# Kernel tuning notes

Measured on AMD Instinct MI355X. Metric: run time of the kernel, lower is better.

The kernel has to match this reference:

```python
import jax, jax.numpy as jnp
import numpy as np

D = 256      # d_model
NH = 8       # num_heads
NP = 4       # n_points
H = 100      # feature map height (single level)
W = 100      # feature map width
B = 4
Q = H * W
S = H * W


def setup_inputs() -> dict:
    key = jax.random.key(0)
    ks = jax.random.split(key, 12)
    p = lambda k, shp, s=0.02: jax.random.normal(k, shp, jnp.float32) * s
    return {
        "hidden_states": jax.random.normal(ks[0], (B, Q, D), jnp.float32),
        "encoder_hidden_states": jax.random.normal(ks[1], (B, S, D), jnp.float32),
        "reference_points": jax.random.uniform(ks[2], (B, Q, 1, 2), jnp.float32),
        "spatial_shapes": jnp.array([[H, W]], dtype=jnp.int32),
        "W_off": p(ks[3], (NH * NP * 2, D)),
        "b_off": p(ks[4], (NH * NP * 2,), 0.5),
        "W_attn": p(ks[5], (NH * NP, D)),
        "b_attn": jnp.zeros((NH * NP,), jnp.float32),
        "W_val": p(ks[6], (D, D)),
        "b_val": jnp.zeros((D,), jnp.float32),
        "W_out": p(ks[7], (D, D)),
        "b_out": jnp.zeros((D,), jnp.float32),
    }


def _deform_attn(hidden_states, encoder_hidden_states, reference_points,
                 W_off, b_off, W_attn, b_attn, W_val, b_val, W_out, b_out):
    Bsz, Qn, Dm = hidden_states.shape
    d = Dm // NH

    # value projection -> [B, NH, S, d]
    value = (encoder_hidden_states @ W_val.T + b_val).reshape(Bsz, S, NH, d)
    vflat = value.transpose(0, 2, 1, 3).reshape(Bsz * NH, H * W, d)

    # sampling offsets [B,Q,NH,NP,2] (n_levels=1 squeezed)
    off = (hidden_states @ W_off.T + b_off).reshape(Bsz, Qn, NH, NP, 2)
    # attention weights softmax over (n_levels*n_points)=NP -> [B,Q,NH,NP]
    attn = jax.nn.softmax((hidden_states @ W_attn.T + b_attn).reshape(Bsz, Qn, NH, NP), axis=-1)

    # normalized sampling locations: ref + off / [W, H]
    normalizer = jnp.array([W, H], jnp.float32)
    # reference_points: [B,Q,1,2] (level dim) -> broadcast over heads/points
    loc = reference_points[:, :, None, 0, None, :] + off / normalizer  # [B,Q,NH,NP,2]

    # grid_sample semantics: grid = 2*loc - 1, align_corners=False, zeros padding
    gx = 2.0 * loc[..., 0] - 1.0
    gy = 2.0 * loc[..., 1] - 1.0
    x = ((gx + 1.0) * W - 1.0) * 0.5   # pixel coords [B,Q,NH,NP]
    y = ((gy + 1.0) * H - 1.0) * 0.5
    x0 = jnp.floor(x); y0 = jnp.floor(y)
    x1 = x0 + 1.0;     y1 = y0 + 1.0
    wx1 = x - x0; wx0 = 1.0 - wx1
    wy1 = y - y0; wy0 = 1.0 - wy1

    bh = jnp.arange(Bsz * NH)[:, None]

    def corner(xi, yi, wgt):
        valid = (xi >= 0) & (xi <= W - 1) & (yi >= 0) & (yi <= H - 1)
        xi_c = jnp.clip(xi, 0, W - 1).astype(jnp.int32)
        yi_c = jnp.clip(yi, 0, H - 1).astype(jnp.int32)
        idx = (yi_c * W + xi_c).transpose(0, 2, 1, 3).reshape(Bsz * NH, Qn * NP)
        g = vflat[bh, idx]  # [B*NH, Q*NP, d]
        wv = (wgt * valid.astype(wgt.dtype)).transpose(0, 2, 1, 3).reshape(Bsz * NH, Qn * NP, 1)
        return g * wv

    sampled = corner(x0, y0, wx0 * wy0)
    sampled = sampled + corner(x1, y0, wx1 * wy0)
    sampled = sampled + corner(x0, y1, wx0 * wy1)
    sampled = sampled + corner(x1, y1, wx1 * wy1)
    sampled = sampled.reshape(Bsz, NH, Qn, NP, d)

    out = jnp.einsum("bhqpd,bqhp->bqhd", sampled, attn).reshape(Bsz, Qn, Dm)
    return out @ W_out.T + b_out


def reference(hidden_states, encoder_hidden_states, reference_points, spatial_shapes,
              W_off, b_off, W_attn, b_attn, W_val, b_val, W_out, b_out):
    # spatial_shapes is static metadata (must equal [[H, W]]); shapes are baked in.
    return _deform_attn(hidden_states, encoder_hidden_states, reference_points,
                        W_off, b_off, W_attn, b_attn, W_val, b_val, W_out, b_out)
```

## Files before the change

kernel.cpp:

```cpp
#include <hip/hip_runtime.h>

constexpr int HH = 100;
constexpr int WW = 100;
constexpr int NH = 8;
constexpr int NP = 4;
constexpr int B  = 4;
constexpr int Q  = HH * WW;
constexpr int S  = Q;
constexpr int K  = 256;
constexpr int DH = 32;
constexpr int M  = B * Q;
constexpr int NTILES = M / 32;

typedef __attribute__((ext_vector_type(8))) short short8;
typedef __attribute__((ext_vector_type(4))) float f32x4;

struct __align__(8) ushort4p { unsigned short x, y, z, w; };

__device__ inline unsigned short f2bf(float f) {
    unsigned u = __builtin_bit_cast(unsigned, f);
    u += 0x7fffu + ((u >> 16) & 1u);
    return (unsigned short)(u >> 16);
}
__device__ inline float bf2f(unsigned short h) {
    return __builtin_bit_cast(float, ((unsigned)h) << 16);
}
__device__ inline unsigned short f2h(float f) {
    _Float16 h = (_Float16)f;
    return __builtin_bit_cast(unsigned short, h);
}
__device__ inline float h2f(unsigned short u) {
    return (float)__builtin_bit_cast(_Float16, u);
}

__device__ inline void lds_st16s(short* base, int row, int stride, int kcol, short8 v) {
    *reinterpret_cast<short8*>(&base[row * stride + (kcol ^ ((row & 7) << 3))]) = v;
}
__device__ inline short8 lds_ld16s(const short* base, int row, int stride, int kcol) {
    return *reinterpret_cast<const short8*>(&base[row * stride + (kcol ^ ((row & 7) << 3))]);
}

__device__ inline short8 cvt8(float4 a, float4 b) {
    short8 r;
    r[0] = (short)f2bf(a.x); r[1] = (short)f2bf(a.y);
    r[2] = (short)f2bf(a.z); r[3] = (short)f2bf(a.w);
    r[4] = (short)f2bf(b.x); r[5] = (short)f2bf(b.y);
    r[6] = (short)f2bf(b.z); r[7] = (short)f2bf(b.w);
    return r;
}

__global__ __launch_bounds__(1024) void stage1(
    const float* __restrict__ enc, const float* __restrict__ Wval,
    const float* __restrict__ bval, unsigned short* __restrict__ vflat,
    const float* __restrict__ hidden, const float* __restrict__ Woff,
    const float* __restrict__ Wattn, const float* __restrict__ boff,
    const float* __restrict__ battn, unsigned short* __restrict__ proj)
{
    __shared__ __align__(16) short As[2][32 * 256];

    const int tid  = threadIdx.x;
    const int lane = tid & 63, w = tid >> 6;
    const int l15  = lane & 15, l4 = lane >> 4;
    const int arow = tid >> 5, ak = (tid & 31) * 8;

    constexpr int NV = 143, NJ = 113;

    if (blockIdx.x < NV) {
        const int n = w * 16 + l15;
        short8 breg[8];
#pragma unroll
        for (int ks = 0; ks < 8; ++ks) {
            const float* s = &Wval[(size_t)n * K + ks * 32 + l4 * 8];
            breg[ks] = cvt8(*reinterpret_cast<const float4*>(s),
                            *reinterpret_cast<const float4*>(s + 4));
        }
        const int nbase = w * 16 + l4 * 4;
        const float4 bias4 = *reinterpret_cast<const float4*>(&bval[nbase]);
        const int h = w >> 1;
        const int dd0 = nbase & 31;

        int t = blockIdx.x;
        float4 fa0, fa1;
        auto lda = [&](int tt) {
            const float* s = &enc[(size_t)(tt * 32 + arow) * K + ak];
            fa0 = *reinterpret_cast<const float4*>(s);
            fa1 = *reinterpret_cast<const float4*>(s + 4);
        };
        lda(t);
        lds_st16s(As[0], arow, 256, ak, cvt8(fa0, fa1));
        __syncthreads();
        int cur = 0;
        for (; t < NTILES; t += NV) {
            const bool more = (t + NV < NTILES);
            if (more) lda(t + NV);

            f32x4 acc0 = {0.f, 0.f, 0.f, 0.f}, acc1 = {0.f, 0.f, 0.f, 0.f};
#pragma unroll
            for (int ks = 0; ks < 8; ++ks) {
                const int kc = ks * 32 + l4 * 8;
                const short8 a0 = lds_ld16s(As[cur], l15, 256, kc);
                const short8 a1 = lds_ld16s(As[cur], 16 + l15, 256, kc);
                acc0 = __builtin_amdgcn_mfma_f32_16x16x32_bf16(breg[ks], a0, acc0, 0, 0, 0);
                acc1 = __builtin_amdgcn_mfma_f32_16x16x32_bf16(breg[ks], a1, acc1, 0, 0, 0);
            }
            const int m0 = t * 32;
            {
                const int m = m0 + l15;
                const int b_ = m / S, s_ = m - b_ * S;
                ushort4p pk;
                pk.x = f2bf(acc0[0] + bias4.x);
                pk.y = f2bf(acc0[1] + bias4.y);
                pk.z = f2bf(acc0[2] + bias4.z);
                pk.w = f2bf(acc0[3] + bias4.w);
                *reinterpret_cast<ushort4p*>(
                    &vflat[(((size_t)(b_ * NH + h)) * S + s_) * DH + dd0]) = pk;
            }
            {
                const int m = m0 + 16 + l15;
                const int b_ = m / S, s_ = m - b_ * S;
                ushort4p pk;
                pk.x = f2bf(acc1[0] + bias4.x);
                pk.y = f2bf(acc1[1] + bias4.y);
                pk.z = f2bf(acc1[2] + bias4.z);
                pk.w = f2bf(acc1[3] + bias4.w);
                *reinterpret_cast<ushort4p*>(
                    &vflat[(((size_t)(b_ * NH + h)) * S + s_) * DH + dd0]) = pk;
            }
            if (more) lds_st16s(As[cur ^ 1], arow, 256, ak, cvt8(fa0, fa1));
            __syncthreads();
            cur ^= 1;
        }
    } else {
        const int nf = w >> 1, mh = w & 1;
        const int n = nf * 16 + l15;
        short8 breg[8];
        float4 bias4 = {0.f, 0.f, 0.f, 0.f};
        const int nbase = nf * 16 + l4 * 4;
        if (w < 12) {
#pragma unroll
            for (int ks = 0; ks < 8; ++ks) {
                const float* s = (n < 64)
                    ? &Woff[(size_t)n * K + ks * 32 + l4 * 8]
                    : &Wattn[(size_t)(n - 64) * K + ks * 32 + l4 * 8];
                breg[ks] = cvt8(*reinterpret_cast<const float4*>(s),
                                *reinterpret_cast<const float4*>(s + 4));
            }
            bias4 = (nf < 4)
                ? *reinterpret_cast<const float4*>(&boff[nbase])
                : *reinterpret_cast<const float4*>(&battn[nbase - 64]);
        }

        int t = blockIdx.x - NV;
        float4 fa0, fa1;
        auto lda = [&](int tt) {
            const float* s = &hidden[(size_t)(tt * 32 + arow) * K + ak];
            fa0 = *reinterpret_cast<const float4*>(s);
            fa1 = *reinterpret_cast<const float4*>(s + 4);
        };
        lda(t);
        lds_st16s(As[0], arow, 256, ak, cvt8(fa0, fa1));
        __syncthreads();
        int cur = 0;
        for (; t < NTILES; t += NJ) {
            const bool more = (t + NJ < NTILES);
            if (more) lda(t + NJ);

            if (w < 12) {
                f32x4 acc = {0.f, 0.f, 0.f, 0.f};
#pragma unroll
                for (int ks = 0; ks < 8; ++ks) {
                    const int kc = ks * 32 + l4 * 8;
                    const short8 a = lds_ld16s(As[cur], mh * 16 + l15, 256, kc);
                    acc = __builtin_amdgcn_mfma_f32_16x16x32_bf16(breg[ks], a, acc, 0, 0, 0);
                }
                const int m = t * 32 + mh * 16 + l15;
                ushort4p pk;
                pk.x = f2h(acc[0] + bias4.x);
                pk.y = f2h(acc[1] + bias4.y);
                pk.z = f2h(acc[2] + bias4.z);
                pk.w = f2h(acc[3] + bias4.w);
                *reinterpret_cast<ushort4p*>(&proj[(size_t)m * 96 + nbase]) = pk;
            }
            if (more) lds_st16s(As[cur ^ 1], arow, 256, ak, cvt8(fa0, fa1));
            __syncthreads();
            cur ^= 1;
        }
    }
}

__global__ __launch_bounds__(256) void sample_agg(
    const unsigned short* __restrict__ vflat,
    const unsigned short* __restrict__ proj,
    const float* __restrict__ ref,
    unsigned short* __restrict__ tmp)
{
    const int nblk = gridDim.x;
    const int cpx  = nblk >> 3;
    const int swz  = (blockIdx.x & 7) * cpx + (blockIdx.x >> 3);

    const int lg   = threadIdx.x >> 2;
    const int lane = threadIdx.x & 3;
    const int d0   = lane * 8;

    const int g  = swz * 64 + lg;
    const int q  = g % Q;
    const int bh = g / Q;
    const int b  = bh >> 3;
    const int h  = bh & 7;

    const size_t bq = (size_t)b * Q + q;
    const float refx = ref[bq * 2 + 0];
    const float refy = ref[bq * 2 + 1];
    const unsigned short* pr = proj + bq * 96;

    float l[NP];
#pragma unroll
    for (int p = 0; p < NP; ++p) l[p] = h2f(pr[64 + h * 4 + p]);
    const float mx = fmaxf(fmaxf(l[0], l[1]), fmaxf(l[2], l[3]));
    float e[NP];
    float esum = 0.f;
#pragma unroll
    for (int p = 0; p < NP; ++p) { e[p] = __expf(l[p] - mx); esum += e[p]; }
    const float inv = 1.f / esum;

    const unsigned short* vbase = vflat + (size_t)bh * (S * DH);

    int   cidx[NP][4];
    float cw[NP][4];
#pragma unroll
    for (int p = 0; p < NP; ++p) {
        const float ox = h2f(pr[h * 8 + p * 2 + 0]);
        const float oy = h2f(pr[h * 8 + p * 2 + 1]);
        const float x = fmaf(refx, (float)WW, ox) - 0.5f;
        const float y = fmaf(refy, (float)HH, oy) - 0.5f;
        const float x0f = floorf(x), y0f = floorf(y);
        const float wx1 = x - x0f, wx0 = 1.f - wx1;
        const float wy1 = y - y0f, wy0 = 1.f - wy1;
        const int x0 = (int)x0f, y0 = (int)y0f;
        const bool vx0 = (x0 >= 0) && (x0 < WW);
        const bool vx1 = (x0 + 1 >= 0) && (x0 + 1 < WW);
        const bool vy0 = (y0 >= 0) && (y0 < HH);
        const bool vy1 = (y0 + 1 >= 0) && (y0 + 1 < HH);
        const int xi0 = min(max(x0, 0), WW - 1);
        const int xi1 = min(max(x0 + 1, 0), WW - 1);
        const int yi0 = min(max(y0, 0), HH - 1);
        const int yi1 = min(max(y0 + 1, 0), HH - 1);
        const float ap = e[p] * inv;
        cw[p][0] = ap * wx0 * wy0 * ((vx0 && vy0) ? 1.f : 0.f);
        cw[p][1] = ap * wx1 * wy0 * ((vx1 && vy0) ? 1.f : 0.f);
        cw[p][2] = ap * wx0 * wy1 * ((vx0 && vy1) ? 1.f : 0.f);
        cw[p][3] = ap * wx1 * wy1 * ((vx1 && vy1) ? 1.f : 0.f);
        cidx[p][0] = (yi0 * WW + xi0) * DH + d0;
        cidx[p][1] = (yi0 * WW + xi1) * DH + d0;
        cidx[p][2] = (yi1 * WW + xi0) * DH + d0;
        cidx[p][3] = (yi1 * WW + xi1) * DH + d0;
    }

    float o[8];
#pragma unroll
    for (int j = 0; j < 8; ++j) o[j] = 0.f;
#pragma unroll
    for (int p = 0; p < NP; ++p) {
#pragma unroll
        for (int c = 0; c < 4; ++c) {
            const short8 v = *reinterpret_cast<const short8*>(&vbase[cidx[p][c]]);
            const float wgt = cw[p][c];
#pragma unroll
            for (int j = 0; j < 8; ++j)
                o[j] = fmaf(wgt, bf2f((unsigned short)v[j]), o[j]);
        }
    }

    short8 ov;
#pragma unroll
    for (int j = 0; j < 8; ++j) ov[j] = (short)f2bf(o[j]);
    *reinterpret_cast<short8*>(&tmp[bq * 256 + h * 32 + d0]) = ov;
}

__global__ __launch_bounds__(1024) void out_proj(
    const unsigned short* __restrict__ tmp, const float* __restrict__ Wo,
    const float* __restrict__ bo, float* __restrict__ out)
{
    __shared__ __align__(16) short As[2][32 * 256];

    const int tid  = threadIdx.x;
    const int lane = tid & 63, w = tid >> 6;
    const int l15  = lane & 15, l4 = lane >> 4;
    const int arow = tid >> 5, ak = (tid & 31) * 8;

    const int n = w * 16 + l15;
    short8 breg[8];
#pragma unroll
    for (int ks = 0; ks < 8; ++ks) {
        const float* s = &Wo[(size_t)n * K + ks * 32 + l4 * 8];
        breg[ks] = cvt8(*reinterpret_cast<const float4*>(s),
                        *reinterpret_cast<const float4*>(s + 4));
    }
    const int nbase = w * 16 + l4 * 4;
    const float4 bias4 = *reinterpret_cast<const float4*>(&bo[nbase]);

    int t = blockIdx.x;
    short8 sa;
    auto lda = [&](int tt) {
        sa = *reinterpret_cast<const short8*>(&tmp[(size_t)(tt * 32 + arow) * K + ak]);
    };
    lda(t);
    lds_st16s(As[0], arow, 256, ak, sa);
    __syncthreads();
    int cur = 0;
    for (; t < NTILES; t += 256) {
        const bool more = (t + 256 < NTILES);
        if (more) lda(t + 256);

        f32x4 acc0 = {0.f, 0.f, 0.f, 0.f}, acc1 = {0.f, 0.f, 0.f, 0.f};
#pragma unroll
        for (int ks = 0; ks < 8; ++ks) {
            const int kc = ks * 32 + l4 * 8;
            const short8 a0 = lds_ld16s(As[cur], l15, 256, kc);
            const short8 a1 = lds_ld16s(As[cur], 16 + l15, 256, kc);
            acc0 = __builtin_amdgcn_mfma_f32_16x16x32_bf16(breg[ks], a0, acc0, 0, 0, 0);
            acc1 = __builtin_amdgcn_mfma_f32_16x16x32_bf16(breg[ks], a1, acc1, 0, 0, 0);
        }
        const int m0 = t * 32;
        {
            const int m = m0 + l15;
            float4 pv;
            pv.x = acc0[0] + bias4.x; pv.y = acc0[1] + bias4.y;
            pv.z = acc0[2] + bias4.z; pv.w = acc0[3] + bias4.w;
            *reinterpret_cast<float4*>(&out[(size_t)m * K + nbase]) = pv;
        }
        {
            const int m = m0 + 16 + l15;
            float4 pv;
            pv.x = acc1[0] + bias4.x; pv.y = acc1[1] + bias4.y;
            pv.z = acc1[2] + bias4.z; pv.w = acc1[3] + bias4.w;
            *reinterpret_cast<float4*>(&out[(size_t)m * K + nbase]) = pv;
        }
        if (more) lds_st16s(As[cur ^ 1], arow, 256, ak, sa);
        __syncthreads();
        cur ^= 1;
    }
}

extern "C" void kernel_launch(void* const* d_in, const int* in_sizes, int n_in,
                              void* d_out, int out_size, void* d_ws, size_t ws_size,
                              hipStream_t stream)
{
    const float* hidden = (const float*)d_in[0];
    const float* enc    = (const float*)d_in[1];
    const float* refp   = (const float*)d_in[2];
    const float* W_off  = (const float*)d_in[4];
    const float* b_off  = (const float*)d_in[5];
    const float* W_attn = (const float*)d_in[6];
    const float* b_attn = (const float*)d_in[7];
    const float* W_val  = (const float*)d_in[8];
    const float* b_val  = (const float*)d_in[9];
    const float* W_out  = (const float*)d_in[10];
    const float* b_out  = (const float*)d_in[11];
    float* out = (float*)d_out;

    unsigned short* vflat = (unsigned short*)d_ws;
    unsigned short* proj  = vflat + (size_t)10240000;
    unsigned short* tmp   = proj + (size_t)3840000;

    stage1<<<256, 1024, 0, stream>>>(
        enc, W_val, b_val, vflat, hidden, W_off, W_attn, b_off, b_attn, proj);

    sample_agg<<<5000, 256, 0, stream>>>(vflat, proj, refp, tmp);

    out_proj<<<256, 1024, 0, stream>>>(tmp, W_out, b_out, out);
}
```

Measured before the change: 71.95 us.

## Stage GEMM input tiles via async global-to-LDS loads with four-deep buffering

Replaces the register-staged double-buffered A-tile loads in the projection and output GEMM kernels with direct global_load_lds transfers into four rotating LDS buffers, prefetching three tiles ahead. The barriers are driven by explicit vmcnt waits. In stage1 the fp32 activations now sit in LDS and are converted to bf16 when fragments are read, using an XOR-swizzled layout. The aim is to hide global memory latency and remove the register round trip. In exchange stage1 needs a large LDS footprint, roughly 128KB, which limits occupancy, and correctness depends on hand-counted vmcnt values that also cover in-flight stores.

New measurement: 91.27 us. 1.27x slower.

```diff
diff --git a/kernel.cpp b/kernel.cpp
--- a/kernel.cpp
+++ b/kernel.cpp
@@ -49,6 +49,11 @@
     return r;
 }
 
+#define GLDS(srcp, dstp) \
+    __builtin_amdgcn_global_load_lds( \
+        (const __attribute__((address_space(1))) unsigned int*)(srcp), \
+        (__attribute__((address_space(3))) unsigned int*)(dstp), 16, 0, 0)
+
 __global__ __launch_bounds__(1024) void stage1(
     const float* __restrict__ enc, const float* __restrict__ Wval,
     const float* __restrict__ bval, unsigned short* __restrict__ vflat,
@@ -56,14 +61,26 @@
     const float* __restrict__ Wattn, const float* __restrict__ boff,
     const float* __restrict__ battn, unsigned short* __restrict__ proj)
 {
-    __shared__ __align__(16) short As[2][32 * 256];
+    __shared__ __align__(16) float fbuf[4][32 * 256];
 
     const int tid  = threadIdx.x;
     const int lane = tid & 63, w = tid >> 6;
     const int l15  = lane & 15, l4 = lane >> 4;
-    const int arow = tid >> 5, ak = (tid & 31) * 8;
 
     constexpr int NV = 143, NJ = 113;
+
+    const int r0 = 2 * w, r1 = 2 * w + 1;
+    const int sc0 = lane ^ (r0 & 7);
+    const int sc1 = lane ^ (r1 & 7);
+
+    auto ldfrag = [&](const float* buf, int r, int ks) -> short8 {
+        const int c0 = ks * 8 + l4 * 2;
+        const float4 p0 = *reinterpret_cast<const float4*>(
+            &buf[r * 256 + ((c0 ^ (r & 7)) << 2)]);
+        const float4 p1 = *reinterpret_cast<const float4*>(
+            &buf[r * 256 + (((c0 + 1) ^ (r & 7)) << 2)]);
+        return cvt8(p0, p1);
+    };
 
     if (blockIdx.x < NV) {
         const int n = w * 16 + l15;
@@ -78,28 +95,27 @@
         const float4 bias4 = *reinterpret_cast<const float4*>(&bval[nbase]);
         const int h = w >> 1;
         const int dd0 = nbase & 31;
+        asm volatile("s_waitcnt vmcnt(0)" ::: "memory");
+
+        auto stage = [&](int tt, int bi) {
+            GLDS(enc + (size_t)(tt * 32 + r0) * K + sc0 * 4, &fbuf[bi][r0 * 256]);
+            GLDS(enc + (size_t)(tt * 32 + r1) * K + sc1 * 4, &fbuf[bi][r1 * 256]);
+        };
 
         int t = blockIdx.x;
-        float4 fa0, fa1;
-        auto lda = [&](int tt) {
-            const float* s = &enc[(size_t)(tt * 32 + arow) * K + ak];
-            fa0 = *reinterpret_cast<const float4*>(s);
-            fa1 = *reinterpret_cast<const float4*>(s + 4);
-        };
-        lda(t);
-        lds_st16s(As[0], arow, 256, ak, cvt8(fa0, fa1));
-        __syncthreads();
-        int cur = 0;
-        for (; t < NTILES; t += NV) {
-            const bool more = (t + NV < NTILES);
-            if (more) lda(t + NV);
-
+        stage(t, 0);
+        if (t + NV < NTILES) stage(t + NV, 1);
+        if (t + 2 * NV < NTILES) stage(t + 2 * NV, 2);
+        asm volatile("s_waitcnt vmcnt(4)\ns_barrier" ::: "memory");
+
+        int bi = 0;
+        for (; t < NTILES; t += NV, bi = (bi + 1) & 3) {
+            const float* buf = fbuf[bi];
             f32x4 acc0 = {0.f, 0.f, 0.f, 0.f}, acc1 = {0.f, 0.f, 0.f, 0.f};
 #pragma unroll
             for (int ks = 0; ks < 8; ++ks) {
-                const int kc = ks * 32 + l4 * 8;
-                const short8 a0 = lds_ld16s(As[cur], l15, 256, kc);
-                const short8 a1 = lds_ld16s(As[cur], 16 + l15, 256, kc);
+                const short8 a0 = ldfrag(buf, l15, ks);
+                const short8 a1 = ldfrag(buf, 16 + l15, ks);
                 acc0 = __builtin_amdgcn_mfma_f32_16x16x32_bf16(breg[ks], a0, acc0, 0, 0, 0);
                 acc1 = __builtin_amdgcn_mfma_f32_16x16x32_bf16(breg[ks], a1, acc1, 0, 0, 0);
             }
@@ -126,9 +142,12 @@
                 *reinterpret_cast<ushort4p*>(
                     &vflat[(((size_t)(b_ * NH + h)) * S + s_) * DH + dd0]) = pk;
             }
-            if (more) lds_st16s(As[cur ^ 1], arow, 256, ak, cvt8(fa0, fa1));
-            __syncthreads();
-            cur ^= 1;
+            if (t + 3 * NV < NTILES) {
+                stage(t + 3 * NV, (bi + 3) & 3);
+                asm volatile("s_waitcnt vmcnt(4)\ns_barrier" ::: "memory");
+            } else {
+                asm volatile("s_waitcnt vmcnt(2)\ns_barrier" ::: "memory");
+            }
         }
     } else {
         const int nf = w >> 1, mh = w & 1;
@@ -149,28 +168,27 @@
                 ? *reinterpret_cast<const float4*>(&boff[nbase])
                 : *reinterpret_cast<const float4*>(&battn[nbase - 64]);
         }
+        asm volatile("s_waitcnt vmcnt(0)" ::: "memory");
+
+        auto stage = [&](int tt, int bi) {
+            GLDS(hidden + (size_t)(tt * 32 + r0) * K + sc0 * 4, &fbuf[bi][r0 * 256]);
+            GLDS(hidden + (size_t)(tt * 32 + r1) * K + sc1 * 4, &fbuf[bi][r1 * 256]);
+        };
 
         int t = blockIdx.x - NV;
-        float4 fa0, fa1;
-        auto lda = [&](int tt) {
-            const float* s = &hidden[(size_t)(tt * 32 + arow) * K + ak];
-            fa0 = *reinterpret_cast<const float4*>(s);
-            fa1 = *reinterpret_cast<const float4*>(s + 4);
-        };
-        lda(t);
-        lds_st16s(As[0], arow, 256, ak, cvt8(fa0, fa1));
-        __syncthreads();
-        int cur = 0;
-        for (; t < NTILES; t += NJ) {
-            const bool more = (t + NJ < NTILES);
-            if (more) lda(t + NJ);
-
+        stage(t, 0);
+        if (t + NJ < NTILES) stage(t + NJ, 1);
+        if (t + 2 * NJ < NTILES) stage(t + 2 * NJ, 2);
+        asm volatile("s_waitcnt vmcnt(4)\ns_barrier" ::: "memory");
+
+        int bi = 0;
+        for (; t < NTILES; t += NJ, bi = (bi + 1) & 3) {
+            const float* buf = fbuf[bi];
             if (w < 12) {
                 f32x4 acc = {0.f, 0.f, 0.f, 0.f};
 #pragma unroll
                 for (int ks = 0; ks < 8; ++ks) {
-                    const int kc = ks * 32 + l4 * 8;
-                    const short8 a = lds_ld16s(As[cur], mh * 16 + l15, 256, kc);
+                    const short8 a = ldfrag(buf, mh * 16 + l15, ks);
                     acc = __builtin_amdgcn_mfma_f32_16x16x32_bf16(breg[ks], a, acc, 0, 0, 0);
                 }
                 const int m = t * 32 + mh * 16 + l15;
@@ -181,9 +199,12 @@
                 pk.w = f2h(acc[3] + bias4.w);
                 *reinterpret_cast<ushort4p*>(&proj[(size_t)m * 96 + nbase]) = pk;
             }
-            if (more) lds_st16s(As[cur ^ 1], arow, 256, ak, cvt8(fa0, fa1));
-            __syncthreads();
-            cur ^= 1;
+            if (t + 3 * NJ < NTILES) {
+                stage(t + 3 * NJ, (bi + 3) & 3);
+                asm volatile("s_waitcnt vmcnt(4)\ns_barrier" ::: "memory");
+            } else {
+                asm volatile("s_waitcnt vmcnt(2)\ns_barrier" ::: "memory");
+            }
         }
     }
 }
@@ -281,12 +302,11 @@
     const unsigned short* __restrict__ tmp, const float* __restrict__ Wo,
     const float* __restrict__ bo, float* __restrict__ out)
 {
-    __shared__ __align__(16) short As[2][32 * 256];
+    __shared__ __align__(16) short bbuf[4][32 * 256];
 
     const int tid  = threadIdx.x;
     const int lane = tid & 63, w = tid >> 6;
     const int l15  = lane & 15, l4 = lane >> 4;
-    const int arow = tid >> 5, ak = (tid & 31) * 8;
 
     const int n = w * 16 + l15;
     short8 breg[8];
@@ -298,26 +318,29 @@
     }
     const int nbase = w * 16 + l4 * 4;
     const float4 bias4 = *reinterpret_cast<const float4*>(&bo[nbase]);
+    asm volatile("s_waitcnt vmcnt(0)" ::: "memory");
+
+    const int srow = 2 * w + (lane >> 5);
+    const int schunk = (lane & 31) ^ (srow & 7);
+    auto stage = [&](int tt, int bi) {
+        GLDS(tmp + (size_t)(tt * 32 + srow) * K + schunk * 8, &bbuf[bi][w * 512]);
+    };
 
     int t = blockIdx.x;
-    short8 sa;
-    auto lda = [&](int tt) {
-        sa = *reinterpret_cast<const short8*>(&tmp[(size_t)(tt * 32 + arow) * K + ak]);
-    };
-    lda(t);
-    lds_st16s(As[0], arow, 256, ak, sa);
-    __syncthreads();
-    int cur = 0;
-    for (; t < NTILES; t += 256) {
-        const bool more = (t + 256 < NTILES);
-        if (more) lda(t + 256);
-
+    stage(t, 0);
+    if (t + 256 < NTILES) stage(t + 256, 1);
+    if (t + 512 < NTILES) stage(t + 512, 2);
+    asm volatile("s_waitcnt vmcnt(2)\ns_barrier" ::: "memory");
+
+    int bi = 0;
+    for (; t < NTILES; t += 256, bi = (bi + 1) & 3) {
+        const short* buf = bbuf[bi];
         f32x4 acc0 = {0.f, 0.f, 0.f, 0.f}, acc1 = {0.f, 0.f, 0.f, 0.f};
 #pragma unroll
         for (int ks = 0; ks < 8; ++ks) {
             const int kc = ks * 32 + l4 * 8;
-            const short8 a0 = lds_ld16s(As[cur], l15, 256, kc);
-            const short8 a1 = lds_ld16s(As[cur], 16 + l15, 256, kc);
+            const short8 a0 = lds_ld16s(buf, l15, 256, kc);
+            const short8 a1 = lds_ld16s(buf, 16 + l15, 256, kc);
             acc0 = __builtin_amdgcn_mfma_f32_16x16x32_bf16(breg[ks], a0, acc0, 0, 0, 0);
             acc1 = __builtin_amdgcn_mfma_f32_16x16x32_bf16(breg[ks], a1, acc1, 0, 0, 0);
         }
@@ -336,9 +359,12 @@
             pv.z = acc1[2] + bias4.z; pv.w = acc1[3] + bias4.w;
             *reinterpret_cast<float4*>(&out[(size_t)m * K + nbase]) = pv;
         }
-        if (more) lds_st16s(As[cur ^ 1], arow, 256, ak, sa);
-        __syncthreads();
-        cur ^= 1;
+        if (t + 768 < NTILES) {
+            stage(t + 768, (bi + 3) & 3);
+            asm volatile("s_waitcnt vmcnt(4)\ns_barrier" ::: "memory");
+        } else {
+            asm volatile("s_waitcnt vmcnt(2)\ns_barrier" ::: "memory");
+        }
     }
 }
 
```

## Stage weights in LDS and stream activation rows per wave without block syncs

Applied to the files above, without the earlier changes.

The projection GEMM in stage1 is restructured so that each block loads the full converted weight matrix (256x256 bf16 for the value projection, 96x256 for offsets and attention) into LDS once. Each wave then independently streams a 16-row activation tile from global memory into registers and loops over all output column chunks, reading B fragments from LDS. This removes the per-tile shared A double buffer and the block-wide __syncthreads. In exchange it uses 128KB of LDS per block, re-reads B from LDS for every row tile, and drops the explicit prefetch of the next A tile.

Result: slower. 134.5 us (+86.9%).

```diff
diff --git a/kernel.cpp b/kernel.cpp
--- a/kernel.cpp
+++ b/kernel.cpp
@@ -11,6 +11,7 @@
 constexpr int DH = 32;
 constexpr int M  = B * Q;
 constexpr int NTILES = M / 32;
+constexpr int T16 = M / 16;
 
 typedef __attribute__((ext_vector_type(8))) short short8;
 typedef __attribute__((ext_vector_type(4))) float f32x4;
@@ -56,134 +57,109 @@
     const float* __restrict__ Wattn, const float* __restrict__ boff,
     const float* __restrict__ battn, unsigned short* __restrict__ proj)
 {
-    __shared__ __align__(16) short As[2][32 * 256];
+    __shared__ __align__(16) short Bs[256 * 256];
 
     const int tid  = threadIdx.x;
     const int lane = tid & 63, w = tid >> 6;
     const int l15  = lane & 15, l4 = lane >> 4;
-    const int arow = tid >> 5, ak = (tid & 31) * 8;
 
     constexpr int NV = 143, NJ = 113;
 
     if (blockIdx.x < NV) {
-        const int n = w * 16 + l15;
-        short8 breg[8];
-#pragma unroll
-        for (int ks = 0; ks < 8; ++ks) {
-            const float* s = &Wval[(size_t)n * K + ks * 32 + l4 * 8];
-            breg[ks] = cvt8(*reinterpret_cast<const float4*>(s),
-                            *reinterpret_cast<const float4*>(s + 4));
-        }
-        const int nbase = w * 16 + l4 * 4;
-        const float4 bias4 = *reinterpret_cast<const float4*>(&bval[nbase]);
-        const int h = w >> 1;
-        const int dd0 = nbase & 31;
-
-        int t = blockIdx.x;
-        float4 fa0, fa1;
-        auto lda = [&](int tt) {
-            const float* s = &enc[(size_t)(tt * 32 + arow) * K + ak];
-            fa0 = *reinterpret_cast<const float4*>(s);
-            fa1 = *reinterpret_cast<const float4*>(s + 4);
-        };
-        lda(t);
-        lds_st16s(As[0], arow, 256, ak, cvt8(fa0, fa1));
+        {
+            const int brow = tid >> 2, kb = (tid & 3) * 64;
+#pragma unroll
+            for (int c = 0; c < 8; ++c) {
+                const float* s = &Wval[(size_t)brow * 256 + kb + c * 8];
+                lds_st16s(Bs, brow, 256, kb + c * 8,
+                          cvt8(*reinterpret_cast<const float4*>(s),
+                               *reinterpret_cast<const float4*>(s + 4)));
+            }
+        }
         __syncthreads();
-        int cur = 0;
-        for (; t < NTILES; t += NV) {
-            const bool more = (t + NV < NTILES);
-            if (more) lda(t + NV);
-
-            f32x4 acc0 = {0.f, 0.f, 0.f, 0.f}, acc1 = {0.f, 0.f, 0.f, 0.f};
+
+        const int nwaves = NV * 16;
+        for (int t = blockIdx.x * 16 + w; t < T16; t += nwaves) {
+            const int mrow = t * 16 + l15;
+            const float* abase = enc + (size_t)mrow * K;
+            short8 areg[8];
 #pragma unroll
             for (int ks = 0; ks < 8; ++ks) {
-                const int kc = ks * 32 + l4 * 8;
-                const short8 a0 = lds_ld16s(As[cur], l15, 256, kc);
-                const short8 a1 = lds_ld16s(As[cur], 16 + l15, 256, kc);
-                acc0 = __builtin_amdgcn_mfma_f32_16x16x32_bf16(breg[ks], a0, acc0, 0, 0, 0);
-                acc1 = __builtin_amdgcn_mfma_f32_16x16x32_bf16(breg[ks], a1, acc1, 0, 0, 0);
-            }
-            const int m0 = t * 32;
-            {
-                const int m = m0 + l15;
-                const int b_ = m / S, s_ = m - b_ * S;
+                const float* s = abase + ks * 32 + l4 * 8;
+                areg[ks] = cvt8(*reinterpret_cast<const float4*>(s),
+                                *reinterpret_cast<const float4*>(s + 4));
+            }
+            const int b_ = mrow / S, s_ = mrow - b_ * S;
+            const size_t obase = ((size_t)b_ * NH) * S + s_;
+
+#pragma unroll 4
+            for (int nc = 0; nc < 16; ++nc) {
+                f32x4 acc = {0.f, 0.f, 0.f, 0.f};
+#pragma unroll
+                for (int ks = 0; ks < 8; ++ks) {
+                    const short8 bb = lds_ld16s(Bs, nc * 16 + l15, 256, ks * 32 + l4 * 8);
+                    acc = __builtin_amdgcn_mfma_f32_16x16x32_bf16(bb, areg[ks], acc, 0, 0, 0);
+                }
+                const int n0 = nc * 16 + l4 * 4;
+                const float4 b4 = *reinterpret_cast<const float4*>(&bval[n0]);
+                const int h = n0 >> 5, dd0 = n0 & 31;
                 ushort4p pk;
-                pk.x = f2bf(acc0[0] + bias4.x);
-                pk.y = f2bf(acc0[1] + bias4.y);
-                pk.z = f2bf(acc0[2] + bias4.z);
-                pk.w = f2bf(acc0[3] + bias4.w);
+                pk.x = f2bf(acc[0] + b4.x);
+                pk.y = f2bf(acc[1] + b4.y);
+                pk.z = f2bf(acc[2] + b4.z);
+                pk.w = f2bf(acc[3] + b4.w);
                 *reinterpret_cast<ushort4p*>(
-                    &vflat[(((size_t)(b_ * NH + h)) * S + s_) * DH + dd0]) = pk;
-            }
-            {
-                const int m = m0 + 16 + l15;
-                const int b_ = m / S, s_ = m - b_ * S;
+                    &vflat[(obase + (size_t)h * S) * DH + dd0]) = pk;
+            }
+        }
+    } else {
+        {
+#pragma unroll
+            for (int j = 0; j < 3; ++j) {
+                const int ch = tid * 3 + j;
+                const int brow = ch >> 5, kc = (ch & 31) * 8;
+                const float* s = (brow < 64)
+                    ? &Woff[(size_t)brow * 256 + kc]
+                    : &Wattn[(size_t)(brow - 64) * 256 + kc];
+                lds_st16s(Bs, brow, 256, kc,
+                          cvt8(*reinterpret_cast<const float4*>(s),
+                               *reinterpret_cast<const float4*>(s + 4)));
+            }
+        }
+        __syncthreads();
+
+        const int nwaves = NJ * 16;
+        for (int t = (blockIdx.x - NV) * 16 + w; t < T16; t += nwaves) {
+            const int mrow = t * 16 + l15;
+            const float* abase = hidden + (size_t)mrow * K;
+            short8 areg[8];
+#pragma unroll
+            for (int ks = 0; ks < 8; ++ks) {
+                const float* s = abase + ks * 32 + l4 * 8;
+                areg[ks] = cvt8(*reinterpret_cast<const float4*>(s),
+                                *reinterpret_cast<const float4*>(s + 4));
+            }
+            const size_t prow = (size_t)mrow * 96;
+
+#pragma unroll
+            for (int nc = 0; nc < 6; ++nc) {
+                f32x4 acc = {0.f, 0.f, 0.f, 0.f};
+#pragma unroll
+                for (int ks = 0; ks < 8; ++ks) {
+                    const short8 bb = lds_ld16s(Bs, nc * 16 + l15, 256, ks * 32 + l4 * 8);
+                    acc = __builtin_amdgcn_mfma_f32_16x16x32_bf16(bb, areg[ks], acc, 0, 0, 0);
+                }
+                const int n0 = nc * 16 + l4 * 4;
+                const float4 b4 = (n0 < 64)
+                    ? *reinterpret_cast<const float4*>(&boff[n0])
+                    : *reinterpret_cast<const float4*>(&battn[n0 - 64]);
                 ushort4p pk;
-                pk.x = f2bf(acc1[0] + bias4.x);
-                pk.y = f2bf(acc1[1] + bias4.y);
-                pk.z = f2bf(acc1[2] + bias4.z);
-                pk.w = f2bf(acc1[3] + bias4.w);
-                *reinterpret_cast<ushort4p*>(
-                    &vflat[(((size_t)(b_ * NH + h)) * S + s_) * DH + dd0]) = pk;
-            }
-            if (more) lds_st16s(As[cur ^ 1], arow, 256, ak, cvt8(fa0, fa1));
-            __syncthreads();
-            cur ^= 1;
-        }
-    } else {
-        const int nf = w >> 1, mh = w & 1;
-        const int n = nf * 16 + l15;
-        short8 breg[8];
-        float4 bias4 = {0.f, 0.f, 0.f, 0.f};
-        const int nbase = nf * 16 + l4 * 4;
-        if (w < 12) {
-#pragma unroll
-            for (int ks = 0; ks < 8; ++ks) {
-                const float* s = (n < 64)
-                    ? &Woff[(size_t)n * K + ks * 32 + l4 * 8]
-                    : &Wattn[(size_t)(n - 64) * K + ks * 32 + l4 * 8];
-                breg[ks] = cvt8(*reinterpret_cast<const float4*>(s),
-                                *reinterpret_cast<const float4*>(s + 4));
-            }
-            bias4 = (nf < 4)
-                ? *reinterpret_cast<const float4*>(&boff[nbase])
-                : *reinterpret_cast<const float4*>(&battn[nbase - 64]);
-        }
-
-        int t = blockIdx.x - NV;
-        float4 fa0, fa1;
-        auto lda = [&](int tt) {
-            const float* s = &hidden[(size_t)(tt * 32 + arow) * K + ak];
-            fa0 = *reinterpret_cast<const float4*>(s);
-            fa1 = *reinterpret_cast<const float4*>(s + 4);
-        };
-        lda(t);
-        lds_st16s(As[0], arow, 256, ak, cvt8(fa0, fa1));
-        __syncthreads();
-        int cur = 0;
-        for (; t < NTILES; t += NJ) {
-            const bool more = (t + NJ < NTILES);
-            if (more) lda(t + NJ);
-
-            if (w < 12) {
-                f32x4 acc = {0.f, 0.f, 0.f, 0.f};
-#pragma unroll
-                for (int ks = 0; ks < 8; ++ks) {
-                    const int kc = ks * 32 + l4 * 8;
-                    const short8 a = lds_ld16s(As[cur], mh * 16 + l15, 256, kc);
-                    acc = __builtin_amdgcn_mfma_f32_16x16x32_bf16(breg[ks], a, acc, 0, 0, 0);
-                }
-                const int m = t * 32 + mh * 16 + l15;
-                ushort4p pk;
-                pk.x = f2h(acc[0] + bias4.x);
-                pk.y = f2h(acc[1] + bias4.y);
-                pk.z = f2h(acc[2] + bias4.z);
-                pk.w = f2h(acc[3] + bias4.w);
-                *reinterpret_cast<ushort4p*>(&proj[(size_t)m * 96 + nbase]) = pk;
-            }
-            if (more) lds_st16s(As[cur ^ 1], arow, 256, ak, cvt8(fa0, fa1));
-            __syncthreads();
-            cur ^= 1;
+                pk.x = f2h(acc[0] + b4.x);
+                pk.y = f2h(acc[1] + b4.y);
+                pk.z = f2h(acc[2] + b4.z);
+                pk.w = f2h(acc[3] + b4.w);
+                *reinterpret_cast<ushort4p*>(&proj[prow + n0]) = pk;
+            }
         }
     }
 }
```

## Halve stage1 block size, give each wave two N-fragments and double grid

Applied to the files above, without the earlier changes.

Stage1 now runs with 512-thread blocks and a 512-block grid instead of 1024 threads and 256 blocks. In the value GEMM each wave now holds two 16-column weight fragments, one full head of 32 columns, and computes a 2x2 MFMA tile, so each LDS A load feeds twice as many MFMAs. In the offset/attention GEMM branch each wave now covers both 16-row halves of a tile. Each thread loads two A rows per tile. The aim is more resident blocks per CU through launch_bounds(512,4) and better register reuse, at the cost of higher register pressure from the doubled B fragments.

Measured after the change: 89.57 us. 24.5% more time.

```diff
diff --git a/kernel.cpp b/kernel.cpp
--- a/kernel.cpp
+++ b/kernel.cpp
@@ -49,7 +49,7 @@
     return r;
 }
 
-__global__ __launch_bounds__(1024) void stage1(
+__global__ __launch_bounds__(512, 4) void stage1(
     const float* __restrict__ enc, const float* __restrict__ Wval,
     const float* __restrict__ bval, unsigned short* __restrict__ vflat,
     const float* __restrict__ hidden, const float* __restrict__ Woff,
@@ -61,127 +61,160 @@
     const int tid  = threadIdx.x;
     const int lane = tid & 63, w = tid >> 6;
     const int l15  = lane & 15, l4 = lane >> 4;
-    const int arow = tid >> 5, ak = (tid & 31) * 8;
-
-    constexpr int NV = 143, NJ = 113;
+    const int ar0 = tid >> 5;
+    const int ar1 = 16 + ar0;
+    const int ak  = (tid & 31) * 8;
+
+    constexpr int NV = 286, NJ = 226;
 
     if (blockIdx.x < NV) {
-        const int n = w * 16 + l15;
-        short8 breg[8];
-#pragma unroll
-        for (int ks = 0; ks < 8; ++ks) {
-            const float* s = &Wval[(size_t)n * K + ks * 32 + l4 * 8];
-            breg[ks] = cvt8(*reinterpret_cast<const float4*>(s),
-                            *reinterpret_cast<const float4*>(s + 4));
-        }
-        const int nbase = w * 16 + l4 * 4;
-        const float4 bias4 = *reinterpret_cast<const float4*>(&bval[nbase]);
-        const int h = w >> 1;
-        const int dd0 = nbase & 31;
+        short8 breg[2][8];
+#pragma unroll
+        for (int j = 0; j < 2; ++j) {
+            const int row = w * 32 + j * 16 + l15;
+#pragma unroll
+            for (int ks = 0; ks < 8; ++ks) {
+                const float* s = &Wval[(size_t)row * K + ks * 32 + l4 * 8];
+                breg[j][ks] = cvt8(*reinterpret_cast<const float4*>(s),
+                                   *reinterpret_cast<const float4*>(s + 4));
+            }
+        }
+        const int n00 = w * 32 + l4 * 4;
+        const int n01 = n00 + 16;
+        const float4 b40 = *reinterpret_cast<const float4*>(&bval[n00]);
+        const float4 b41 = *reinterpret_cast<const float4*>(&bval[n01]);
+        const int dd0 = n00 & 31, dd1 = n01 & 31;
 
         int t = blockIdx.x;
-        float4 fa0, fa1;
+        float4 f00, f01, f10, f11;
         auto lda = [&](int tt) {
-            const float* s = &enc[(size_t)(tt * 32 + arow) * K + ak];
-            fa0 = *reinterpret_cast<const float4*>(s);
-            fa1 = *reinterpret_cast<const float4*>(s + 4);
+            const float* s0 = &enc[(size_t)(tt * 32 + ar0) * K + ak];
+            f00 = *reinterpret_cast<const float4*>(s0);
+            f01 = *reinterpret_cast<const float4*>(s0 + 4);
+            const float* s1 = &enc[(size_t)(tt * 32 + ar1) * K + ak];
+            f10 = *reinterpret_cast<const float4*>(s1);
+            f11 = *reinterpret_cast<const float4*>(s1 + 4);
+        };
+        auto wr = [&](short* dst) {
+            lds_st16s(dst, ar0, 256, ak, cvt8(f00, f01));
+            lds_st16s(dst, ar1, 256, ak, cvt8(f10, f11));
         };
         lda(t);
-        lds_st16s(As[0], arow, 256, ak, cvt8(fa0, fa1));
+        wr(As[0]);
         __syncthreads();
         int cur = 0;
         for (; t < NTILES; t += NV) {
             const bool more = (t + NV < NTILES);
             if (more) lda(t + NV);
 
-            f32x4 acc0 = {0.f, 0.f, 0.f, 0.f}, acc1 = {0.f, 0.f, 0.f, 0.f};
+            f32x4 acc[2][2];
+#pragma unroll
+            for (int i = 0; i < 2; ++i)
+#pragma unroll
+                for (int j = 0; j < 2; ++j) acc[i][j] = f32x4{0.f, 0.f, 0.f, 0.f};
 #pragma unroll
             for (int ks = 0; ks < 8; ++ks) {
                 const int kc = ks * 32 + l4 * 8;
                 const short8 a0 = lds_ld16s(As[cur], l15, 256, kc);
                 const short8 a1 = lds_ld16s(As[cur], 16 + l15, 256, kc);
-                acc0 = __builtin_amdgcn_mfma_f32_16x16x32_bf16(breg[ks], a0, acc0, 0, 0, 0);
-                acc1 = __builtin_amdgcn_mfma_f32_16x16x32_bf16(breg[ks], a1, acc1, 0, 0, 0);
+                acc[0][0] = __builtin_amdgcn_mfma_f32_16x16x32_bf16(breg[0][ks], a0, acc[0][0], 0, 0, 0);
+                acc[0][1] = __builtin_amdgcn_mfma_f32_16x16x32_bf16(breg[1][ks], a0, acc[0][1], 0, 0, 0);
+                acc[1][0] = __builtin_amdgcn_mfma_f32_16x16x32_bf16(breg[0][ks], a1, acc[1][0], 0, 0, 0);
+                acc[1][1] = __builtin_amdgcn_mfma_f32_16x16x32_bf16(breg[1][ks], a1, acc[1][1], 0, 0, 0);
             }
-            const int m0 = t * 32;
-            {
-                const int m = m0 + l15;
+#pragma unroll
+            for (int mf = 0; mf < 2; ++mf) {
+                const int m = t * 32 + mf * 16 + l15;
                 const int b_ = m / S, s_ = m - b_ * S;
-                ushort4p pk;
-                pk.x = f2bf(acc0[0] + bias4.x);
-                pk.y = f2bf(acc0[1] + bias4.y);
-                pk.z = f2bf(acc0[2] + bias4.z);
-                pk.w = f2bf(acc0[3] + bias4.w);
-                *reinterpret_cast<ushort4p*>(
-                    &vflat[(((size_t)(b_ * NH + h)) * S + s_) * DH + dd0]) = pk;
+                const size_t obase = (((size_t)(b_ * NH + w)) * S + s_) * DH;
+                ushort4p p0;
+                p0.x = f2bf(acc[mf][0][0] + b40.x);
+                p0.y = f2bf(acc[mf][0][1] + b40.y);
+                p0.z = f2bf(acc[mf][0][2] + b40.z);
+                p0.w = f2bf(acc[mf][0][3] + b40.w);
+                *reinterpret_cast<ushort4p*>(&vflat[obase + dd0]) = p0;
+                ushort4p p1;
+                p1.x = f2bf(acc[mf][1][0] + b41.x);
+                p1.y = f2bf(acc[mf][1][1] + b41.y);
+                p1.z = f2bf(acc[mf][1][2] + b41.z);
+                p1.w = f2bf(acc[mf][1][3] + b41.w);
+                *reinterpret_cast<ushort4p*>(&vflat[obase + dd1]) = p1;
             }
-            {
-                const int m = m0 + 16 + l15;
-                const int b_ = m / S, s_ = m - b_ * S;
-                ushort4p pk;
-                pk.x = f2bf(acc1[0] + bias4.x);
-                pk.y = f2bf(acc1[1] + bias4.y);
-                pk.z = f2bf(acc1[2] + bias4.z);
-                pk.w = f2bf(acc1[3] + bias4.w);
-                *reinterpret_cast<ushort4p*>(
-                    &vflat[(((size_t)(b_ * NH + h)) * S + s_) * DH + dd0]) = pk;
-            }
-            if (more) lds_st16s(As[cur ^ 1], arow, 256, ak, cvt8(fa0, fa1));
+            if (more) wr(As[cur ^ 1]);
             __syncthreads();
             cur ^= 1;
         }
     } else {
-        const int nf = w >> 1, mh = w & 1;
-        const int n = nf * 16 + l15;
         short8 breg[8];
         float4 bias4 = {0.f, 0.f, 0.f, 0.f};
-        const int nbase = nf * 16 + l4 * 4;
-        if (w < 12) {
+        const int n0 = w * 16 + l4 * 4;
+        if (w < 6) {
+            const int row = w * 16 + l15;
 #pragma unroll
             for (int ks = 0; ks < 8; ++ks) {
-                const float* s = (n < 64)
-                    ? &Woff[(size_t)n * K + ks * 32 + l4 * 8]
-                    : &Wattn[(size_t)(n - 64) * K + ks * 32 + l4 * 8];
+                const float* s = (row < 64)
+                    ? &Woff[(size_t)row * K + ks * 32 + l4 * 8]
+                    : &Wattn[(size_t)(row - 64) * K + ks * 32 + l4 * 8];
                 breg[ks] = cvt8(*reinterpret_cast<const float4*>(s),
                                 *reinterpret_cast<const float4*>(s + 4));
             }
-            bias4 = (nf < 4)
-                ? *reinterpret_cast<const float4*>(&boff[nbase])
-                : *reinterpret_cast<const float4*>(&battn[nbase - 64]);
+            bias4 = (n0 < 64)
+                ? *reinterpret_cast<const float4*>(&boff[n0])
+                : *reinterpret_cast<const float4*>(&battn[n0 - 64]);
         }
 
         int t = blockIdx.x - NV;
-        float4 fa0, fa1;
+        float4 f00, f01, f10, f11;
         auto lda = [&](int tt) {
-            const float* s = &hidden[(size_t)(tt * 32 + arow) * K + ak];
-            fa0 = *reinterpret_cast<const float4*>(s);
-            fa1 = *reinterpret_cast<const float4*>(s + 4);
+            const float* s0 = &hidden[(size_t)(tt * 32 + ar0) * K + ak];
+            f00 = *reinterpret_cast<const float4*>(s0);
+            f01 = *reinterpret_cast<const float4*>(s0 + 4);
+            const float* s1 = &hidden[(size_t)(tt * 32 + ar1) * K + ak];
+            f10 = *reinterpret_cast<const float4*>(s1);
+            f11 = *reinterpret_cast<const float4*>(s1 + 4);
+        };
+        auto wr = [&](short* dst) {
+            lds_st16s(dst, ar0, 256, ak, cvt8(f00, f01));
+            lds_st16s(dst, ar1, 256, ak, cvt8(f10, f11));
         };
         lda(t);
-        lds_st16s(As[0], arow, 256, ak, cvt8(fa0, fa1));
+        wr(As[0]);
         __syncthreads();
         int cur = 0;
         for (; t < NTILES; t += NJ) {
             const bool more = (t + NJ < NTILES);
             if (more) lda(t + NJ);
 
-            if (w < 12) {
-                f32x4 acc = {0.f, 0.f, 0.f, 0.f};
+            if (w < 6) {
+                f32x4 acc0 = {0.f, 0.f, 0.f, 0.f}, acc1 = {0.f, 0.f, 0.f, 0.f};
 #pragma unroll
                 for (int ks = 0; ks < 8; ++ks) {
                     const int kc = ks * 32 + l4 * 8;
-                    const short8 a = lds_ld16s(As[cur], mh * 16 + l15, 256, kc);
-                    acc = __builtin_amdgcn_mfma_f32_16x16x32_bf16(breg[ks], a, acc, 0, 0, 0);
+                    const short8 a0 = lds_ld16s(As[cur], l15, 256, kc);
+                    const short8 a1 = lds_ld16s(As[cur], 16 + l15, 256, kc);
+                    acc0 = __builtin_amdgcn_mfma_f32_16x16x32_bf16(breg[ks], a0, acc0, 0, 0, 0);
+                    acc1 = __builtin_amdgcn_mfma_f32_16x16x32_bf16(breg[ks], a1, acc1, 0, 0, 0);
                 }
-                const int m = t * 32 + mh * 16 + l15;
-                ushort4p pk;
-                pk.x = f2h(acc[0] + bias4.x);
-                pk.y = f2h(acc[1] + bias4.y);
-                pk.z = f2h(acc[2] + bias4.z);
-                pk.w = f2h(acc[3] + bias4.w);
-                *reinterpret_cast<ushort4p*>(&proj[(size_t)m * 96 + nbase]) = pk;
+                {
+                    const int m = t * 32 + l15;
+                    ushort4p pk;
+                    pk.x = f2h(acc0[0] + bias4.x);
+                    pk.y = f2h(acc0[1] + bias4.y);
+                    pk.z = f2h(acc0[2] + bias4.z);
+                    pk.w = f2h(acc0[3] + bias4.w);
+                    *reinterpret_cast<ushort4p*>(&proj[(size_t)m * 96 + n0]) = pk;
+                }
+                {
+                    const int m = t * 32 + 16 + l15;
+                    ushort4p pk;
+                    pk.x = f2h(acc1[0] + bias4.x);
+                    pk.y = f2h(acc1[1] + bias4.y);
+                    pk.z = f2h(acc1[2] + bias4.z);
+                    pk.w = f2h(acc1[3] + bias4.w);
+                    *reinterpret_cast<ushort4p*>(&proj[(size_t)m * 96 + n0]) = pk;
+                }
             }
-            if (more) lds_st16s(As[cur ^ 1], arow, 256, ak, cvt8(fa0, fa1));
+            if (more) wr(As[cur ^ 1]);
             __syncthreads();
             cur ^= 1;
         }
@@ -363,7 +396,7 @@
     unsigned short* proj  = vflat + (size_t)10240000;
     unsigned short* tmp   = proj + (size_t)3840000;
 
-    stage1<<<256, 1024, 0, stream>>>(
+    stage1<<<512, 512, 0, stream>>>(
         enc, W_val, b_val, vflat, hidden, W_off, W_attn, b_off, b_attn, proj);
 
     sample_agg<<<5000, 256, 0, stream>>>(vflat, proj, refp, tmp);
```
